# Kernel optimization log

Measured on AMD Instinct MI355X. Metric: run time of the kernel, lower is better.

The kernel has to match this reference:

```python
import jax, jax.numpy as jnp
import numpy as np

B = 768
D = 128
NUM_CLASSES = 32
MARGIN = 1.0
EPS = 1e-12  # avoid sqrt(0) -> nan grad on the diagonal


def setup_inputs() -> dict:
    key = jax.random.key(0)
    k1, k2 = jax.random.split(key)
    embeddings = jax.random.normal(k1, (B, D), dtype=jnp.float32)
    labels = jax.random.randint(k2, (B,), 0, NUM_CLASSES, dtype=jnp.int32)
    return {"embeddings": embeddings, "labels": labels}


def _triplet_loss(embeddings, labels, margin):
    n = embeddings.shape[0]
    # pairwise euclidean distances (torch.cdist p=2)
    sq = jnp.sum(embeddings * embeddings, axis=1)
    d2 = sq[:, None] + sq[None, :] - 2.0 * (embeddings @ embeddings.T)
    d = jnp.sqrt(jnp.maximum(d2, EPS))  # [B, B]

    same = labels[:, None] == labels[None, :]
    eye = jnp.eye(n, dtype=bool)
    pos_mask = same & ~eye          # valid anchor-positive pairs
    neg_mask = ~same                # valid negatives per anchor
    neg_exists = neg_mask.any(axis=1)

    # hardest negative per anchor (argmin over negatives) -- fallback
    d_neg_only = jnp.where(neg_mask, d, jnp.inf)
    hardest = jnp.argmin(d_neg_only, axis=1)  # [B]

    # semi-hard mask[i, j, k]: k is negative of i and pd < d[i,k] < pd + margin
    pd = d[:, :, None]   # d[i, j]
    nd = d[:, None, :]   # d[i, k]
    semi = neg_mask[:, None, :] & (nd > pd) & (nd < pd + margin)  # [B,B,B] bool
    semi_any = semi.any(axis=2)                 # [B, B]
    first_semi = jnp.argmax(semi, axis=2)       # first True index, like negative_indices[mask][0]

    neg_idx = jnp.where(semi_any, first_semi, hardest[:, None])  # [B, B]
    neg_d = jnp.take_along_axis(d, neg_idx, axis=1)              # [B, B]

    valid = pos_mask & neg_exists[:, None]
    per_triplet = jax.nn.relu(d - neg_d + margin)  # relu(pos - neg + margin)
    cnt = jnp.sum(valid)
    loss = jnp.sum(jnp.where(valid, per_triplet, 0.0)) / jnp.maximum(cnt, 1).astype(per_triplet.dtype)
    return loss


def reference(embeddings, labels):
    return _triplet_loss(embeddings, labels, MARGIN)
```

## Files before the change

### kernel.cpp

```cpp
#include <hip/hip_runtime.h>
#include <math.h>

#define NB 768
#define ND 128
#define NC 12
#define APB 4
#define TL_MARGIN 1.0f
#define TL_EPS 1e-12f


__global__ __launch_bounds__(256) void triplet_batch_kernel(
    const float* __restrict__ E, const int* __restrict__ L,
    float* __restrict__ psum, float* __restrict__ pcnt)
{
    __shared__ float arow[APB][ND];
    __shared__ float drows[APB][NB];
    __shared__ int   lbl[NB];
    __shared__ float s_sqi[APB];

    const int i0   = blockIdx.x * APB;
    const int tid  = threadIdx.x;
    const int lane = tid & 63;
    const int wave = tid >> 6;

    for (int j = tid; j < NB; j += 256) lbl[j] = L[j];
    for (int idx = tid; idx < APB * ND; idx += 256) {
        int a = idx >> 7, k = idx & 127;
        arow[a][k] = E[(size_t)(i0 + a) * ND + k];
    }
    __syncthreads();

    {
        float v0 = arow[wave][lane];
        float v1 = arow[wave][lane + 64];
        float s = v0 * v0 + v1 * v1;
        #pragma unroll
        for (int off = 32; off > 0; off >>= 1) s += __shfl_xor(s, off);
        if (lane == 0) s_sqi[wave] = s;
    }
    __syncthreads();
    const float sq0 = s_sqi[0], sq1 = s_sqi[1], sq2 = s_sqi[2], sq3 = s_sqi[3];

    for (int j = tid; j < NB; j += 256) {
        const float4* ej = (const float4*)(E + (size_t)j * ND);
        const float4* a0p = (const float4*)arow[0];
        const float4* a1p = (const float4*)arow[1];
        const float4* a2p = (const float4*)arow[2];
        const float4* a3p = (const float4*)arow[3];
        float d0 = 0.f, d1 = 0.f, d2 = 0.f, d3 = 0.f, sj = 0.f;
        #pragma unroll 8
        for (int k = 0; k < ND / 4; ++k) {
            float4 v  = ej[k];
            float4 a0 = a0p[k], a1 = a1p[k], a2 = a2p[k], a3 = a3p[k];
            sj += v.x * v.x + v.y * v.y + v.z * v.z + v.w * v.w;
            d0 += a0.x * v.x + a0.y * v.y + a0.z * v.z + a0.w * v.w;
            d1 += a1.x * v.x + a1.y * v.y + a1.z * v.z + a1.w * v.w;
            d2 += a2.x * v.x + a2.y * v.y + a2.z * v.z + a2.w * v.w;
            d3 += a3.x * v.x + a3.y * v.y + a3.z * v.z + a3.w * v.w;
        }
        drows[0][j] = sqrtf(fmaxf(sq0 + sj - 2.f * d0, TL_EPS));
        drows[1][j] = sqrtf(fmaxf(sq1 + sj - 2.f * d1, TL_EPS));
        drows[2][j] = sqrtf(fmaxf(sq2 + sj - 2.f * d2, TL_EPS));
        drows[3][j] = sqrtf(fmaxf(sq3 + sj - 2.f * d3, TL_EPS));
    }
    __syncthreads();

    const int a  = wave;
    const int ia = i0 + a;
    const int li = lbl[ia];

    float dk[NC];
    unsigned negm = 0u, posm = 0u;
    #pragma unroll
    for (int c = 0; c < NC; ++c) {
        int j = c * 64 + lane;
        dk[c] = drows[a][j];
        int lj = lbl[j];
        if (lj != li)    negm |= (1u << c);
        else if (j != ia) posm |= (1u << c);
    }

    float bv = INFINITY;
    #pragma unroll
    for (int c = 0; c < NC; ++c)
        if ((negm >> c) & 1u) bv = fminf(bv, dk[c]);
    #pragma unroll
    for (int off = 32; off > 0; off >>= 1)
        bv = fminf(bv, __shfl_xor(bv, off));
    const float hval = bv;

    float lsum = 0.f, lcnt = 0.f;
    if (isfinite(hval)) {
        #pragma unroll 1
        for (int c = 0; c < NC; ++c) {
            unsigned long long pm = __ballot((posm >> c) & 1u);
            while (pm) {
                const int sl = __builtin_ctzll(pm);
                pm &= pm - 1;
                const float pd = __shfl(dk[c], sl);
                float nd = hval;
                #pragma unroll 1
                for (int c2 = 0; c2 < NC; ++c2) {
                    bool pred = ((negm >> c2) & 1u) &&
                                (dk[c2] > pd) && (dk[c2] < pd + TL_MARGIN);
                    unsigned long long m = __ballot(pred);
                    if (m) { nd = __shfl(dk[c2], __builtin_ctzll(m)); break; }
                }
                lsum += fmaxf(pd - nd + TL_MARGIN, 0.f);
                lcnt += 1.f;
            }
        }
    }
    if (lane == 0) { psum[ia] = lsum; pcnt[ia] = lcnt; }
}

__global__ __launch_bounds__(256) void triplet_finalize_kernel(
    const float* __restrict__ psum, const float* __restrict__ pcnt,
    float* __restrict__ out)
{
    __shared__ float sa[256];
    __shared__ float sb[256];
    const int tid = threadIdx.x;
    float a = 0.f, b = 0.f;
    for (int j = tid; j < NB; j += 256) { a += psum[j]; b += pcnt[j]; }
    sa[tid] = a; sb[tid] = b;
    __syncthreads();
    for (int s = 128; s > 0; s >>= 1) {
        if (tid < s) { sa[tid] += sa[tid + s]; sb[tid] += sb[tid + s]; }
        __syncthreads();
    }
    if (tid == 0) out[0] = sa[0] / fmaxf(sb[0], 1.f);
}

extern "C" void kernel_launch(void* const* d_in, const int* in_sizes, int n_in,
                              void* d_out, int out_size, void* d_ws, size_t ws_size,
                              hipStream_t stream) {
    const float* E = (const float*)d_in[0];
    const int*   L = (const int*)d_in[1];
    float* psum = (float*)d_ws;
    float* pcnt = psum + NB;
    float* out  = (float*)d_out;

    triplet_batch_kernel<<<NB / APB, 256, 0, stream>>>(E, L, psum, pcnt);
    triplet_finalize_kernel<<<1, 256, 0, stream>>>(psum, pcnt, out);
}
```

Baseline: 33.41 us.

## Coalesce distance row loads with 16-lane split dot products and wave-level finalize

The distance computation is reorganised so each group of 16 lanes cooperatively reads one embedding row with coalesced float4 loads. Anchor fragments are held in registers, and partial dot products are reduced with xor shuffles. Before, each thread strided through its own row, giving uncoalesced global reads. The finalize kernel is shrunk to a single wavefront that reduces with shuffles instead of shared memory and barriers. The change adds shuffle reduction work and leaves most lanes idle on the final store.

```diff
diff --git a/kernel.cpp b/kernel.cpp
--- a/kernel.cpp
+++ b/kernel.cpp
@@ -39,29 +39,45 @@
         if (lane == 0) s_sqi[wave] = s;
     }
     __syncthreads();
-    const float sq0 = s_sqi[0], sq1 = s_sqi[1], sq2 = s_sqi[2], sq3 = s_sqi[3];
 
-    for (int j = tid; j < NB; j += 256) {
-        const float4* ej = (const float4*)(E + (size_t)j * ND);
-        const float4* a0p = (const float4*)arow[0];
-        const float4* a1p = (const float4*)arow[1];
-        const float4* a2p = (const float4*)arow[2];
-        const float4* a3p = (const float4*)arow[3];
+    const int r = lane >> 4;
+    const int g = lane & 15;
+
+    float4 afr[2][APB];
+    #pragma unroll
+    for (int i = 0; i < 2; ++i)
+        #pragma unroll
+        for (int a = 0; a < APB; ++a)
+            afr[i][a] = *(const float4*)&arow[a][(i * 16 + g) * 4];
+
+    #pragma unroll 4
+    for (int grp = 0; grp < 48; ++grp) {
+        const int j = wave * 192 + grp * 4 + r;
+        const float4* ejp = (const float4*)(E + (size_t)j * ND);
         float d0 = 0.f, d1 = 0.f, d2 = 0.f, d3 = 0.f, sj = 0.f;
-        #pragma unroll 8
-        for (int k = 0; k < ND / 4; ++k) {
-            float4 v  = ej[k];
-            float4 a0 = a0p[k], a1 = a1p[k], a2 = a2p[k], a3 = a3p[k];
+        #pragma unroll
+        for (int i = 0; i < 2; ++i) {
+            float4 v = ejp[i * 16 + g];
             sj += v.x * v.x + v.y * v.y + v.z * v.z + v.w * v.w;
+            float4 a0 = afr[i][0], a1 = afr[i][1], a2 = afr[i][2], a3 = afr[i][3];
             d0 += a0.x * v.x + a0.y * v.y + a0.z * v.z + a0.w * v.w;
             d1 += a1.x * v.x + a1.y * v.y + a1.z * v.z + a1.w * v.w;
             d2 += a2.x * v.x + a2.y * v.y + a2.z * v.z + a2.w * v.w;
             d3 += a3.x * v.x + a3.y * v.y + a3.z * v.z + a3.w * v.w;
         }
-        drows[0][j] = sqrtf(fmaxf(sq0 + sj - 2.f * d0, TL_EPS));
-        drows[1][j] = sqrtf(fmaxf(sq1 + sj - 2.f * d1, TL_EPS));
-        drows[2][j] = sqrtf(fmaxf(sq2 + sj - 2.f * d2, TL_EPS));
-        drows[3][j] = sqrtf(fmaxf(sq3 + sj - 2.f * d3, TL_EPS));
+        #pragma unroll
+        for (int off = 1; off < 16; off <<= 1) {
+            d0 += __shfl_xor(d0, off);
+            d1 += __shfl_xor(d1, off);
+            d2 += __shfl_xor(d2, off);
+            d3 += __shfl_xor(d3, off);
+            sj += __shfl_xor(sj, off);
+        }
+        if (g < APB) {
+            float dsel = (g == 0) ? d0 : (g == 1) ? d1 : (g == 2) ? d2 : d3;
+            float d2v  = s_sqi[g] + sj - 2.f * dsel;
+            drows[g][j] = sqrtf(fmaxf(d2v, TL_EPS));
+        }
     }
     __syncthreads();
 
@@ -76,7 +92,7 @@
         int j = c * 64 + lane;
         dk[c] = drows[a][j];
         int lj = lbl[j];
-        if (lj != li)    negm |= (1u << c);
+        if (lj != li)     negm |= (1u << c);
         else if (j != ia) posm |= (1u << c);
     }
 
@@ -114,22 +130,19 @@
     if (lane == 0) { psum[ia] = lsum; pcnt[ia] = lcnt; }
 }
 
-__global__ __launch_bounds__(256) void triplet_finalize_kernel(
+__global__ __launch_bounds__(64) void triplet_finalize_kernel(
     const float* __restrict__ psum, const float* __restrict__ pcnt,
     float* __restrict__ out)
 {
-    __shared__ float sa[256];
-    __shared__ float sb[256];
-    const int tid = threadIdx.x;
+    const int lane = threadIdx.x;
     float a = 0.f, b = 0.f;
-    for (int j = tid; j < NB; j += 256) { a += psum[j]; b += pcnt[j]; }
-    sa[tid] = a; sb[tid] = b;
-    __syncthreads();
-    for (int s = 128; s > 0; s >>= 1) {
-        if (tid < s) { sa[tid] += sa[tid + s]; sb[tid] += sb[tid + s]; }
-        __syncthreads();
+    for (int j = lane; j < NB; j += 64) { a += psum[j]; b += pcnt[j]; }
+    #pragma unroll
+    for (int off = 32; off > 0; off >>= 1) {
+        a += __shfl_xor(a, off);
+        b += __shfl_xor(b, off);
     }
-    if (tid == 0) out[0] = sa[0] / fmaxf(sb[0], 1.f);
+    if (lane == 0) out[0] = a / fmaxf(b, 1.f);
 }
 
 extern "C" void kernel_launch(void* const* d_in, const int* in_sizes, int n_in,
@@ -142,5 +155,5 @@
     float* out  = (float*)d_out;
 
     triplet_batch_kernel<<<NB / APB, 256, 0, stream>>>(E, L, psum, pcnt);
-    triplet_finalize_kernel<<<1, 256, 0, stream>>>(psum, pcnt, out);
+    triplet_finalize_kernel<<<1, 64, 0, stream>>>(psum, pcnt, out);
 }
```

Result: slower. 47.28 us (+41.5%).
